# Kernel tuning notes

Hardware: AMD Instinct MI355X
Metric: run time of the kernel (lower is better)

Reference implementation:

```python
import jax, jax.numpy as jnp
import numpy as np

P_DROP = 0.25
DROP_KEY_SEED = 42  # fixed seed makes dropout deterministic for baseline comparison


def setup_inputs() -> dict:
    key = jax.random.key(0)
    k1, k2, k3, k4 = jax.random.split(key, 4)
    B, S, D, DV = 16, 2048, 64, 512
    x1 = jax.random.normal(k1, (B, S, D), dtype=jnp.float32)   # queries [B,S,64]
    m = jax.random.normal(k2, (D, DV), dtype=jnp.float32)      # [64,512]
    n = jax.random.normal(k3, (S, DV), dtype=jnp.float32)      # [S,512]
    q = jax.random.normal(k4, (S, DV), dtype=jnp.float32)      # values [S,512]
    return {"x1": x1, "m": m, "n": n, "q": q}


def reference(x1, m, n, q):
    scale = jnp.float32(1.0 / 64.0)  # hard-coded in original (not 1/sqrt(d))
    kT = jnp.matmul(m, n.T)                        # matmul5: [64, S]
    scores = jnp.matmul(x1, kT) * scale            # [B, S, S]
    probs = jax.nn.softmax(scores, axis=-1)        # softmax over last dim
    keep = jax.random.bernoulli(jax.random.key(DROP_KEY_SEED), 1.0 - P_DROP, probs.shape)
    probs = jnp.where(keep, probs / (1.0 - P_DROP), jnp.float32(0.0))  # dropout (train mode)
    return jnp.matmul(probs, q)                    # [B, S, DV]
```

## Files before the change

### kernel.cpp

```cpp
#include <hip/hip_runtime.h>


typedef short  s8v __attribute__((ext_vector_type(8)));
typedef float  f4v __attribute__((ext_vector_type(4)));

__device__ __forceinline__ unsigned short f2bf(float f) {
  unsigned int u = __float_as_uint(f);
  u += 0x7fffu + ((u >> 16) & 1u);
  return (unsigned short)(u >> 16);
}
__device__ __forceinline__ float bf2f(unsigned short h) {
  return __uint_as_float(((unsigned int)h) << 16);
}

__device__ __forceinline__ unsigned int rotl(unsigned int x, unsigned int r) {
  return __builtin_amdgcn_alignbit(x, x, 32u - r);
}

__device__ __forceinline__ unsigned int jax_bits(unsigned int idx) {
  const unsigned int K0 = 0u, K1 = 42u, K2 = 0x1BD11BDAu ^ K0 ^ K1;
  unsigned int x0 = 0u, x1 = idx;
  x0 += K0; x1 += K1;
#define TF_R(r) { x0 += x1; x1 = rotl(x1, r); x1 ^= x0; }
  TF_R(13) TF_R(15) TF_R(26) TF_R(6)
  x0 += K1; x1 += K2 + 1u;
  TF_R(17) TF_R(29) TF_R(16) TF_R(24)
  x0 += K2; x1 += K0 + 2u;
  TF_R(13) TF_R(15) TF_R(26) TF_R(6)
  x0 += K0; x1 += K1 + 3u;
  TF_R(17) TF_R(29) TF_R(16) TF_R(24)
  x0 += K1; x1 += K2 + 4u;
  TF_R(13) TF_R(15) TF_R(26) TF_R(6)
  x0 += K2; x1 += K0 + 5u;
#undef TF_R
  return x0 ^ x1;
}

__device__ __forceinline__ f4v mfma16(s8v a, s8v b, f4v c) {
  return __builtin_amdgcn_mfma_f32_16x16x32_bf16(a, b, c, 0, 0, 0);
}

__global__ void prep_all(const float* __restrict__ x1, const float* __restrict__ q,
                         const float* __restrict__ m, const float* __restrict__ nmat,
                         unsigned short* __restrict__ Xhi, unsigned short* __restrict__ qT,
                         unsigned short* __restrict__ Khi, unsigned short* __restrict__ Klo) {
  const int blk = blockIdx.x;
  const int t = threadIdx.x;
  if (blk < 512) {
    __shared__ float Lm[64][68];
    const int s = blk * 4 + (t >> 6);
    const int d = t & 63;
    float a0 = 0.f, a1 = 0.f, a2 = 0.f, a3 = 0.f;
    for (int ch = 0; ch < 8; ++ch) {
      const int dv0 = ch * 64;
      __syncthreads();
#pragma unroll
      for (int k = 0; k < 4; ++k) {
        const int fi = t + k * 256;
        const int row = fi >> 4, c4 = fi & 15;
        *(float4*)&Lm[row][c4 * 4] =
            *(const float4*)&m[(size_t)row * 512 + dv0 + c4 * 4];
      }
      __syncthreads();
      const float4* nv = (const float4*)&nmat[(size_t)s * 512 + dv0];
#pragma unroll
      for (int j4 = 0; j4 < 16; ++j4) {
        const float4 nf = nv[j4];
        const float4 mf = *(const float4*)&Lm[d][j4 * 4];
        a0 = fmaf(mf.x, nf.x, a0); a1 = fmaf(mf.y, nf.y, a1);
        a2 = fmaf(mf.z, nf.z, a2); a3 = fmaf(mf.w, nf.w, a3);
      }
    }
    const float kv = ((a0 + a1) + (a2 + a3)) * (1.44269504088896340736f / 64.0f);
    const unsigned short h = f2bf(kv);
    Khi[s * 64 + d] = h;
    Klo[s * 64 + d] = f2bf(kv - bf2f(h));
  } else if (blk < 1536) {
    const int i = ((blk - 512) * 256 + t) * 8;
    float4 a = *(const float4*)&x1[i];
    float4 b = *(const float4*)&x1[i + 4];
    ushort4 o0, o1;
    o0.x = f2bf(a.x); o0.y = f2bf(a.y); o0.z = f2bf(a.z); o0.w = f2bf(a.w);
    o1.x = f2bf(b.x); o1.y = f2bf(b.y); o1.z = f2bf(b.z); o1.w = f2bf(b.w);
    *(ushort4*)&Xhi[i] = o0;
    *(ushort4*)&Xhi[i + 4] = o1;
  } else {
    __shared__ unsigned short tile[64][65];
    const int bb = blk - 1536;
    const int s0 = (bb >> 3) * 64;
    const int d0 = (bb & 7) * 64;
#pragma unroll
    for (int k = 0; k < 16; ++k) {
      int lin = t + k * 256;
      int r = lin >> 6, c = lin & 63;
      tile[c][r] = f2bf(q[(size_t)(s0 + r) * 512 + d0 + c]);
    }
    __syncthreads();
#pragma unroll
    for (int k = 0; k < 16; ++k) {
      int lin = t + k * 256;
      int rr = lin >> 6, cc = lin & 63;
      qT[(size_t)(d0 + rr) * 2048 + s0 + cc] = tile[rr][cc];
    }
  }
}

__global__ __launch_bounds__(512, 4) void attn_main(
    const unsigned short* __restrict__ Xhi,
    const unsigned short* __restrict__ Khi, const unsigned short* __restrict__ Klo,
    const unsigned short* __restrict__ qT, float* __restrict__ out) {
  __shared__ unsigned short Xs[64][72];
  __shared__ unsigned short Ps[2][64][136];
  __shared__ float rsum[8][64];

  const int tid  = threadIdx.x;
  const int wave = tid >> 6;
  const int lane = tid & 63;
  const int l15  = lane & 15;
  const int quad = lane >> 4;

  const int b    = blockIdx.x >> 5;
  const int row0 = (blockIdx.x & 31) * 64;

  {
    const int r = tid >> 3, c8 = (tid & 7) * 8;
    *(uint4*)&Xs[r][c8] =
        *(const uint4*)&Xhi[((size_t)(b * 2048 + row0 + r)) * 64 + c8];
  }

  const unsigned short* __restrict__ khp = Khi + ((wave * 16 + l15) * 64 + quad * 8);
  const unsigned short* __restrict__ klp = Klo + ((wave * 16 + l15) * 64 + quad * 8);
  const unsigned short* __restrict__ qvp = qT + ((wave * 64 + l15) * 2048 + quad * 8);

  s8v Kh0 = *(const s8v*)(khp);
  s8v Kh1 = *(const s8v*)(khp + 32);
  s8v Kl0 = *(const s8v*)(klp);
  s8v Kl1 = *(const s8v*)(klp + 32);

  f4v acc[4][4];
#pragma unroll
  for (int mt = 0; mt < 4; ++mt)
#pragma unroll
    for (int nt = 0; nt < 4; ++nt) acc[mt][nt] = f4v{0.f, 0.f, 0.f, 0.f};
  float rs[4] = {0.f, 0.f, 0.f, 0.f};

  const unsigned int idxl =
      ((unsigned int)(b * 2048 + row0 + l15)) * 2048u +
      (unsigned int)(wave * 16 + quad * 4);

  __syncthreads();

  for (int it = 0; it < 16; ++it) {
    const int kt = it * 128;
    unsigned short (*Pb)[136] = Ps[it & 1];

#pragma unroll
    for (int nt = 0; nt < 4; ++nt) {
      const s8v Xb0 = *(const s8v*)&Xs[nt * 16 + l15][quad * 8];
      const s8v Xb1 = *(const s8v*)&Xs[nt * 16 + l15][quad * 8 + 32];
      f4v c = {0.f, 0.f, 0.f, 0.f};
      c = mfma16(Kh0, Xb0, c);  c = mfma16(Kh1, Xb1, c);
      c = mfma16(Kl0, Xb0, c);  c = mfma16(Kl1, Xb1, c);
      const unsigned int idx0 = idxl + (unsigned int)(nt * 32768 + kt);
      float p[4];
#pragma unroll
      for (int r = 0; r < 4; ++r) {
        float e = exp2f(c[r]);
        rs[nt] += e;
        const unsigned int bits = jax_bits(idx0 + r);
        p[r] = (bits < 0xC0000000u) ? e : 0.0f;
      }
      unsigned int p01, p23;
      asm("v_cvt_pk_bf16_f32 %0, %1, %2" : "=v"(p01) : "v"(p[0]), "v"(p[1]));
      asm("v_cvt_pk_bf16_f32 %0, %1, %2" : "=v"(p23) : "v"(p[2]), "v"(p[3]));
      *(uint2*)&Pb[nt * 16 + l15][wave * 16 + quad * 4] = make_uint2(p01, p23);
    }

    if (it < 15) {
      const int ko = (it + 1) * 8192;
      Kh0 = *(const s8v*)(khp + ko);
      Kh1 = *(const s8v*)(khp + ko + 32);
      Kl0 = *(const s8v*)(klp + ko);
      Kl1 = *(const s8v*)(klp + ko + 32);
    }

    __syncthreads();

#pragma unroll
    for (int ks = 0; ks < 4; ++ks) {
      s8v Va[4];
#pragma unroll
      for (int mt = 0; mt < 4; ++mt)
        Va[mt] = *(const s8v*)(qvp + mt * (16 * 2048) + kt + ks * 32);
      __builtin_amdgcn_s_setprio(1);
#pragma unroll
      for (int nt = 0; nt < 4; ++nt) {
        const s8v Pf = *(const s8v*)&Pb[nt * 16 + l15][ks * 32 + quad * 8];
#pragma unroll
        for (int mt = 0; mt < 4; ++mt) acc[mt][nt] = mfma16(Va[mt], Pf, acc[mt][nt]);
      }
      __builtin_amdgcn_s_setprio(0);
    }
  }

#pragma unroll
  for (int nt = 0; nt < 4; ++nt) {
    float v = rs[nt];
    v += __shfl_xor(v, 16);
    v += __shfl_xor(v, 32);
    if (quad == 0) rsum[wave][nt * 16 + l15] = v;
  }
  __syncthreads();

#pragma unroll
  for (int nt = 0; nt < 4; ++nt) {
    const int rloc = nt * 16 + l15;
    float tot = 0.f;
#pragma unroll
    for (int w2 = 0; w2 < 8; ++w2) tot += rsum[w2][rloc];
    const float inv = 1.0f / (0.75f * tot);
    const size_t base = ((size_t)(b * 2048 + row0 + rloc)) * 512 + wave * 64;
#pragma unroll
    for (int mt = 0; mt < 4; ++mt) {
      f4v v = acc[mt][nt];
      v[0] *= inv; v[1] *= inv; v[2] *= inv; v[3] *= inv;
      *(f4v*)&out[base + mt * 16 + quad * 4] = v;
    }
  }
}

extern "C" void kernel_launch(void* const* d_in, const int* in_sizes, int n_in,
                              void* d_out, int out_size, void* d_ws, size_t ws_size,
                              hipStream_t stream) {
  (void)in_sizes; (void)n_in; (void)out_size; (void)ws_size;
  const float* x1 = (const float*)d_in[0];
  const float* m  = (const float*)d_in[1];
  const float* n  = (const float*)d_in[2];
  const float* q  = (const float*)d_in[3];
  float* out = (float*)d_out;

  char* ws = (char*)d_ws;
  unsigned short* Khi = (unsigned short*)(ws);
  unsigned short* Klo = (unsigned short*)(ws + 262144);
  unsigned short* Xhi = (unsigned short*)(ws + 524288);
  unsigned short* qT  = (unsigned short*)(ws + 4718592);

  prep_all<<<1792, 256, 0, stream>>>(x1, q, m, n, Xhi, qT, Khi, Klo);
  attn_main<<<512, 512, 0, stream>>>(Xhi, Khi, Klo, qT, out);
}
```

Measured before the change: 312.3 us.

## Software-pipeline QK/softmax of next tile with PV of current tile

Restructures the main loop so the score/exp/dropout computation for tile it+1 is issued before the P·V MFMAs of tile it, using the double-buffered P tiles, with a single barrier per iteration. This lets the VALU-heavy Threefry dropout work overlap with the matrix-core work instead of running in separate phases. It also drops the s_setprio hints and replaces __syncthreads with a manual lgkmcnt wait plus barrier and a sched_barrier. The risk is higher register pressure from live K fragments alongside the accumulators, and a redundant K reload on the last iterations.

```diff
diff --git a/kernel.cpp b/kernel.cpp
--- a/kernel.cpp
+++ b/kernel.cpp
@@ -132,11 +132,7 @@
   const unsigned short* __restrict__ klp = Klo + ((wave * 16 + l15) * 64 + quad * 8);
   const unsigned short* __restrict__ qvp = qT + ((wave * 64 + l15) * 2048 + quad * 8);
 
-  s8v Kh0 = *(const s8v*)(khp);
-  s8v Kh1 = *(const s8v*)(khp + 32);
-  s8v Kl0 = *(const s8v*)(klp);
-  s8v Kl1 = *(const s8v*)(klp + 32);
-
+  s8v Kh0, Kh1, Kl0, Kl1;
   f4v acc[4][4];
 #pragma unroll
   for (int mt = 0; mt < 4; ++mt)
@@ -148,12 +144,17 @@
       ((unsigned int)(b * 2048 + row0 + l15)) * 2048u +
       (unsigned int)(wave * 16 + quad * 4);
 
-  __syncthreads();
-
-  for (int it = 0; it < 16; ++it) {
-    const int kt = it * 128;
-    unsigned short (*Pb)[136] = Ps[it & 1];
-
+  auto KLOAD = [&](int itk) {
+    const int ko = itk * 8192;
+    Kh0 = *(const s8v*)(khp + ko);
+    Kh1 = *(const s8v*)(khp + ko + 32);
+    Kl0 = *(const s8v*)(klp + ko);
+    Kl1 = *(const s8v*)(klp + ko + 32);
+  };
+
+  auto QK = [&](int itn) {
+    unsigned short (*Pn)[136] = Ps[itn & 1];
+    const int ktn = itn * 128;
 #pragma unroll
     for (int nt = 0; nt < 4; ++nt) {
       const s8v Xb0 = *(const s8v*)&Xs[nt * 16 + l15][quad * 8];
@@ -161,7 +162,7 @@
       f4v c = {0.f, 0.f, 0.f, 0.f};
       c = mfma16(Kh0, Xb0, c);  c = mfma16(Kh1, Xb1, c);
       c = mfma16(Kl0, Xb0, c);  c = mfma16(Kl1, Xb1, c);
-      const unsigned int idx0 = idxl + (unsigned int)(nt * 32768 + kt);
+      const unsigned int idx0 = idxl + (unsigned int)(nt * 32768 + ktn);
       float p[4];
 #pragma unroll
       for (int r = 0; r < 4; ++r) {
@@ -173,35 +174,47 @@
       unsigned int p01, p23;
       asm("v_cvt_pk_bf16_f32 %0, %1, %2" : "=v"(p01) : "v"(p[0]), "v"(p[1]));
       asm("v_cvt_pk_bf16_f32 %0, %1, %2" : "=v"(p23) : "v"(p[2]), "v"(p[3]));
-      *(uint2*)&Pb[nt * 16 + l15][wave * 16 + quad * 4] = make_uint2(p01, p23);
-    }
-
-    if (it < 15) {
-      const int ko = (it + 1) * 8192;
-      Kh0 = *(const s8v*)(khp + ko);
-      Kh1 = *(const s8v*)(khp + ko + 32);
-      Kl0 = *(const s8v*)(klp + ko);
-      Kl1 = *(const s8v*)(klp + ko + 32);
-    }
-
-    __syncthreads();
-
+      *(uint2*)&Pn[nt * 16 + l15][wave * 16 + quad * 4] = make_uint2(p01, p23);
+    }
+  };
+
+  auto PV = [&](int it) {
+    unsigned short (*Pc)[136] = Ps[it & 1];
+    const int kt = it * 128;
 #pragma unroll
     for (int ks = 0; ks < 4; ++ks) {
       s8v Va[4];
 #pragma unroll
       for (int mt = 0; mt < 4; ++mt)
         Va[mt] = *(const s8v*)(qvp + mt * (16 * 2048) + kt + ks * 32);
-      __builtin_amdgcn_s_setprio(1);
 #pragma unroll
       for (int nt = 0; nt < 4; ++nt) {
-        const s8v Pf = *(const s8v*)&Pb[nt * 16 + l15][ks * 32 + quad * 8];
+        const s8v Pf = *(const s8v*)&Pc[nt * 16 + l15][ks * 32 + quad * 8];
 #pragma unroll
         for (int mt = 0; mt < 4; ++mt) acc[mt][nt] = mfma16(Va[mt], Pf, acc[mt][nt]);
       }
-      __builtin_amdgcn_s_setprio(0);
-    }
-  }
+    }
+  };
+
+  auto bar = [&]() {
+    asm volatile("s_waitcnt lgkmcnt(0)" ::: "memory");
+    __builtin_amdgcn_s_barrier();
+    __builtin_amdgcn_sched_barrier(0);
+  };
+
+  KLOAD(0);
+  __syncthreads();
+  QK(0);
+  KLOAD(1);
+  bar();
+
+  for (int it = 0; it < 15; ++it) {
+    QK(it + 1);
+    KLOAD(it + 2 < 16 ? it + 2 : 15);
+    PV(it);
+    bar();
+  }
+  PV(15);
 
 #pragma unroll
   for (int nt = 0; nt < 4; ++nt) {
```

Result: no change. 317.3 us (+1.6%).

## Precompute dropout bitmask in prep kernel instead of hashing inside attention loop

Applied to the files above, without the earlier changes.

Adds a prep-stage block range that evaluates the Threefry-based dropout RNG for every score element and packs the keep decisions into a 32-bit-per-word bitmask in workspace. The attention kernel then loads one mask word per tile row and tests bits instead of running the 20-round hash inline. This takes heavy integer ALU work and register pressure out of the main loop's critical path. In exchange it adds a 16 MB mask write and read and many more prep blocks.

```diff
diff --git a/kernel.cpp b/kernel.cpp
--- a/kernel.cpp
+++ b/kernel.cpp
@@ -43,7 +43,8 @@
 __global__ void prep_all(const float* __restrict__ x1, const float* __restrict__ q,
                          const float* __restrict__ m, const float* __restrict__ nmat,
                          unsigned short* __restrict__ Xhi, unsigned short* __restrict__ qT,
-                         unsigned short* __restrict__ Khi, unsigned short* __restrict__ Klo) {
+                         unsigned short* __restrict__ Khi, unsigned short* __restrict__ Klo,
+                         unsigned int* __restrict__ mask) {
   const int blk = blockIdx.x;
   const int t = threadIdx.x;
   if (blk < 512) {
@@ -84,7 +85,7 @@
     o1.x = f2bf(b.x); o1.y = f2bf(b.y); o1.z = f2bf(b.z); o1.w = f2bf(b.w);
     *(ushort4*)&Xhi[i] = o0;
     *(ushort4*)&Xhi[i + 4] = o1;
-  } else {
+  } else if (blk < 1792) {
     __shared__ unsigned short tile[64][65];
     const int bb = blk - 1536;
     const int s0 = (bb >> 3) * 64;
@@ -102,13 +103,23 @@
       int rr = lin >> 6, cc = lin & 63;
       qT[(size_t)(d0 + rr) * 2048 + s0 + cc] = tile[rr][cc];
     }
+  } else {
+    const int i = (blk - 1792) * 256 + t;
+    const unsigned int e0 = (unsigned int)i * 32u;
+    unsigned int w = 0u;
+#pragma unroll 4
+    for (int j = 0; j < 32; ++j) {
+      w |= (jax_bits(e0 + (unsigned int)j) < 0xC0000000u ? 1u : 0u) << j;
+    }
+    mask[i] = w;
   }
 }
 
 __global__ __launch_bounds__(512, 4) void attn_main(
     const unsigned short* __restrict__ Xhi,
     const unsigned short* __restrict__ Khi, const unsigned short* __restrict__ Klo,
-    const unsigned short* __restrict__ qT, float* __restrict__ out) {
+    const unsigned short* __restrict__ qT, const unsigned int* __restrict__ mask,
+    float* __restrict__ out) {
   __shared__ unsigned short Xs[64][72];
   __shared__ unsigned short Ps[2][64][136];
   __shared__ float rsum[8][64];
@@ -132,6 +143,11 @@
   const unsigned short* __restrict__ klp = Klo + ((wave * 16 + l15) * 64 + quad * 8);
   const unsigned short* __restrict__ qvp = qT + ((wave * 64 + l15) * 2048 + quad * 8);
 
+  const int wc = wave * 16 + quad * 4;
+  const unsigned int mshift = (unsigned int)(wc & 31);
+  const unsigned int* __restrict__ maskp =
+      mask + ((size_t)(b * 2048 + row0 + l15) * 64 + (wc >> 5));
+
   s8v Kh0 = *(const s8v*)(khp);
   s8v Kh1 = *(const s8v*)(khp + 32);
   s8v Kl0 = *(const s8v*)(klp);
@@ -144,15 +160,16 @@
     for (int nt = 0; nt < 4; ++nt) acc[mt][nt] = f4v{0.f, 0.f, 0.f, 0.f};
   float rs[4] = {0.f, 0.f, 0.f, 0.f};
 
-  const unsigned int idxl =
-      ((unsigned int)(b * 2048 + row0 + l15)) * 2048u +
-      (unsigned int)(wave * 16 + quad * 4);
-
   __syncthreads();
 
   for (int it = 0; it < 16; ++it) {
     const int kt = it * 128;
     unsigned short (*Pb)[136] = Ps[it & 1];
+
+    unsigned int mw[4];
+#pragma unroll
+    for (int nt = 0; nt < 4; ++nt)
+      mw[nt] = maskp[nt * 1024 + it * 4];
 
 #pragma unroll
     for (int nt = 0; nt < 4; ++nt) {
@@ -161,14 +178,12 @@
       f4v c = {0.f, 0.f, 0.f, 0.f};
       c = mfma16(Kh0, Xb0, c);  c = mfma16(Kh1, Xb1, c);
       c = mfma16(Kl0, Xb0, c);  c = mfma16(Kl1, Xb1, c);
-      const unsigned int idx0 = idxl + (unsigned int)(nt * 32768 + kt);
       float p[4];
 #pragma unroll
       for (int r = 0; r < 4; ++r) {
         float e = exp2f(c[r]);
         rs[nt] += e;
-        const unsigned int bits = jax_bits(idx0 + r);
-        p[r] = (bits < 0xC0000000u) ? e : 0.0f;
+        p[r] = ((mw[nt] >> (mshift + r)) & 1u) ? e : 0.0f;
       }
       unsigned int p01, p23;
       asm("v_cvt_pk_bf16_f32 %0, %1, %2" : "=v"(p01) : "v"(p[0]), "v"(p[1]));
@@ -240,11 +255,12 @@
   float* out = (float*)d_out;
 
   char* ws = (char*)d_ws;
-  unsigned short* Khi = (unsigned short*)(ws);
-  unsigned short* Klo = (unsigned short*)(ws + 262144);
-  unsigned short* Xhi = (unsigned short*)(ws + 524288);
-  unsigned short* qT  = (unsigned short*)(ws + 4718592);
-
-  prep_all<<<1792, 256, 0, stream>>>(x1, q, m, n, Xhi, qT, Khi, Klo);
-  attn_main<<<512, 512, 0, stream>>>(Xhi, Khi, Klo, qT, out);
-}
+  unsigned short* Khi  = (unsigned short*)(ws);
+  unsigned short* Klo  = (unsigned short*)(ws + 262144);
+  unsigned short* Xhi  = (unsigned short*)(ws + 524288);
+  unsigned short* qT   = (unsigned short*)(ws + 4718592);
+  unsigned int*   mask = (unsigned int*)(ws + 6815744);
+
+  prep_all<<<9984, 256, 0, stream>>>(x1, q, m, n, Xhi, qT, Khi, Klo, mask);
+  attn_main<<<512, 512, 0, stream>>>(Xhi, Khi, Klo, qT, mask, out);
+}
```

After: 396.7 us. +27.0%, slower.

## Retile attention kernel to 32-row blocks with 4 waves each

Applied to the files above, without the earlier changes.

Halves the query rows per block and the waves per block, doubling the grid, and gives each wave more keys and output columns. Each wave now builds 2 score tiles per key group and accumulates an 8x2 tile of output fragments. The K prefetch across iterations and the staging of V fragments in registers are dropped in favour of loads inside the loop. The intent is more, smaller blocks for better occupancy and balance, at the cost of less reuse of V fragments across query tiles and more exposed load latency.

```diff
diff --git a/kernel.cpp b/kernel.cpp
--- a/kernel.cpp
+++ b/kernel.cpp
@@ -105,13 +105,13 @@
   }
 }
 
-__global__ __launch_bounds__(512, 4) void attn_main(
+__global__ __launch_bounds__(256, 4) void attn_main(
     const unsigned short* __restrict__ Xhi,
     const unsigned short* __restrict__ Khi, const unsigned short* __restrict__ Klo,
     const unsigned short* __restrict__ qT, float* __restrict__ out) {
-  __shared__ unsigned short Xs[64][72];
-  __shared__ unsigned short Ps[2][64][136];
-  __shared__ float rsum[8][64];
+  __shared__ unsigned short Xs[32][72];
+  __shared__ unsigned short Ps[2][32][136];
+  __shared__ float rsum[4][32];
 
   const int tid  = threadIdx.x;
   const int wave = tid >> 6;
@@ -119,8 +119,8 @@
   const int l15  = lane & 15;
   const int quad = lane >> 4;
 
-  const int b    = blockIdx.x >> 5;
-  const int row0 = (blockIdx.x & 31) * 64;
+  const int b    = blockIdx.x >> 6;
+  const int row0 = (blockIdx.x & 63) * 32;
 
   {
     const int r = tid >> 3, c8 = (tid & 7) * 8;
@@ -128,83 +128,79 @@
         *(const uint4*)&Xhi[((size_t)(b * 2048 + row0 + r)) * 64 + c8];
   }
 
-  const unsigned short* __restrict__ khp = Khi + ((wave * 16 + l15) * 64 + quad * 8);
-  const unsigned short* __restrict__ klp = Klo + ((wave * 16 + l15) * 64 + quad * 8);
-  const unsigned short* __restrict__ qvp = qT + ((wave * 64 + l15) * 2048 + quad * 8);
-
-  s8v Kh0 = *(const s8v*)(khp);
-  s8v Kh1 = *(const s8v*)(khp + 32);
-  s8v Kl0 = *(const s8v*)(klp);
-  s8v Kl1 = *(const s8v*)(klp + 32);
-
-  f4v acc[4][4];
-#pragma unroll
-  for (int mt = 0; mt < 4; ++mt)
-#pragma unroll
-    for (int nt = 0; nt < 4; ++nt) acc[mt][nt] = f4v{0.f, 0.f, 0.f, 0.f};
-  float rs[4] = {0.f, 0.f, 0.f, 0.f};
+  const unsigned short* __restrict__ khp0 = Khi + ((wave * 32 + l15) * 64 + quad * 8);
+  const unsigned short* __restrict__ klp0 = Klo + ((wave * 32 + l15) * 64 + quad * 8);
+  const unsigned short* __restrict__ khp1 = khp0 + 16 * 64;
+  const unsigned short* __restrict__ klp1 = klp0 + 16 * 64;
+  const unsigned short* __restrict__ qvp = qT + ((wave * 128 + l15) * 2048 + quad * 8);
+
+  f4v acc[8][2];
+#pragma unroll
+  for (int mt = 0; mt < 8; ++mt)
+#pragma unroll
+    for (int nt = 0; nt < 2; ++nt) acc[mt][nt] = f4v{0.f, 0.f, 0.f, 0.f};
+  float rs[2] = {0.f, 0.f};
 
   const unsigned int idxl =
       ((unsigned int)(b * 2048 + row0 + l15)) * 2048u +
-      (unsigned int)(wave * 16 + quad * 4);
+      (unsigned int)(wave * 32 + quad * 4);
 
   __syncthreads();
 
   for (int it = 0; it < 16; ++it) {
     const int kt = it * 128;
+    const int ko = it * 8192;
     unsigned short (*Pb)[136] = Ps[it & 1];
 
 #pragma unroll
-    for (int nt = 0; nt < 4; ++nt) {
-      const s8v Xb0 = *(const s8v*)&Xs[nt * 16 + l15][quad * 8];
-      const s8v Xb1 = *(const s8v*)&Xs[nt * 16 + l15][quad * 8 + 32];
-      f4v c = {0.f, 0.f, 0.f, 0.f};
-      c = mfma16(Kh0, Xb0, c);  c = mfma16(Kh1, Xb1, c);
-      c = mfma16(Kl0, Xb0, c);  c = mfma16(Kl1, Xb1, c);
-      const unsigned int idx0 = idxl + (unsigned int)(nt * 32768 + kt);
-      float p[4];
-#pragma unroll
-      for (int r = 0; r < 4; ++r) {
-        float e = exp2f(c[r]);
-        rs[nt] += e;
-        const unsigned int bits = jax_bits(idx0 + r);
-        p[r] = (bits < 0xC0000000u) ? e : 0.0f;
-      }
-      unsigned int p01, p23;
-      asm("v_cvt_pk_bf16_f32 %0, %1, %2" : "=v"(p01) : "v"(p[0]), "v"(p[1]));
-      asm("v_cvt_pk_bf16_f32 %0, %1, %2" : "=v"(p23) : "v"(p[2]), "v"(p[3]));
-      *(uint2*)&Pb[nt * 16 + l15][wave * 16 + quad * 4] = make_uint2(p01, p23);
-    }
-
-    if (it < 15) {
-      const int ko = (it + 1) * 8192;
-      Kh0 = *(const s8v*)(khp + ko);
-      Kh1 = *(const s8v*)(khp + ko + 32);
-      Kl0 = *(const s8v*)(klp + ko);
-      Kl1 = *(const s8v*)(klp + ko + 32);
+    for (int kg = 0; kg < 2; ++kg) {
+      const s8v Kh0 = *(const s8v*)((kg ? khp1 : khp0) + ko);
+      const s8v Kh1 = *(const s8v*)((kg ? khp1 : khp0) + ko + 32);
+      const s8v Kl0 = *(const s8v*)((kg ? klp1 : klp0) + ko);
+      const s8v Kl1 = *(const s8v*)((kg ? klp1 : klp0) + ko + 32);
+#pragma unroll
+      for (int nt = 0; nt < 2; ++nt) {
+        const s8v Xb0 = *(const s8v*)&Xs[nt * 16 + l15][quad * 8];
+        const s8v Xb1 = *(const s8v*)&Xs[nt * 16 + l15][quad * 8 + 32];
+        f4v c = {0.f, 0.f, 0.f, 0.f};
+        c = mfma16(Kh0, Xb0, c);  c = mfma16(Kh1, Xb1, c);
+        c = mfma16(Kl0, Xb0, c);  c = mfma16(Kl1, Xb1, c);
+        const unsigned int idx0 =
+            idxl + (unsigned int)(nt * 32768 + kt + kg * 16);
+        float p[4];
+#pragma unroll
+        for (int r = 0; r < 4; ++r) {
+          float e = exp2f(c[r]);
+          rs[nt] += e;
+          const unsigned int bits = jax_bits(idx0 + r);
+          p[r] = (bits < 0xC0000000u) ? e : 0.0f;
+        }
+        unsigned int p01, p23;
+        asm("v_cvt_pk_bf16_f32 %0, %1, %2" : "=v"(p01) : "v"(p[0]), "v"(p[1]));
+        asm("v_cvt_pk_bf16_f32 %0, %1, %2" : "=v"(p23) : "v"(p[2]), "v"(p[3]));
+        *(uint2*)&Pb[nt * 16 + l15][wave * 32 + kg * 16 + quad * 4] =
+            make_uint2(p01, p23);
+      }
     }
 
     __syncthreads();
 
 #pragma unroll
     for (int ks = 0; ks < 4; ++ks) {
-      s8v Va[4];
-#pragma unroll
-      for (int mt = 0; mt < 4; ++mt)
-        Va[mt] = *(const s8v*)(qvp + mt * (16 * 2048) + kt + ks * 32);
-      __builtin_amdgcn_s_setprio(1);
-#pragma unroll
-      for (int nt = 0; nt < 4; ++nt) {
+#pragma unroll
+      for (int nt = 0; nt < 2; ++nt) {
         const s8v Pf = *(const s8v*)&Pb[nt * 16 + l15][ks * 32 + quad * 8];
 #pragma unroll
-        for (int mt = 0; mt < 4; ++mt) acc[mt][nt] = mfma16(Va[mt], Pf, acc[mt][nt]);
-      }
-      __builtin_amdgcn_s_setprio(0);
-    }
-  }
-
-#pragma unroll
-  for (int nt = 0; nt < 4; ++nt) {
+        for (int mt = 0; mt < 8; ++mt) {
+          const s8v Va = *(const s8v*)(qvp + mt * (16 * 2048) + kt + ks * 32);
+          acc[mt][nt] = mfma16(Va, Pf, acc[mt][nt]);
+        }
+      }
+    }
+  }
+
+#pragma unroll
+  for (int nt = 0; nt < 2; ++nt) {
     float v = rs[nt];
     v += __shfl_xor(v, 16);
     v += __shfl_xor(v, 32);
@@ -213,15 +209,13 @@
   __syncthreads();
 
 #pragma unroll
-  for (int nt = 0; nt < 4; ++nt) {
+  for (int nt = 0; nt < 2; ++nt) {
     const int rloc = nt * 16 + l15;
-    float tot = 0.f;
-#pragma unroll
-    for (int w2 = 0; w2 < 8; ++w2) tot += rsum[w2][rloc];
+    const float tot = rsum[0][rloc] + rsum[1][rloc] + rsum[2][rloc] + rsum[3][rloc];
     const float inv = 1.0f / (0.75f * tot);
-    const size_t base = ((size_t)(b * 2048 + row0 + rloc)) * 512 + wave * 64;
-#pragma unroll
-    for (int mt = 0; mt < 4; ++mt) {
+    const size_t base = ((size_t)(b * 2048 + row0 + rloc)) * 512 + wave * 128;
+#pragma unroll
+    for (int mt = 0; mt < 8; ++mt) {
       f4v v = acc[mt][nt];
       v[0] *= inv; v[1] *= inv; v[2] *= inv; v[3] *= inv;
       *(f4v*)&out[base + mt * 16 + quad * 4] = v;
@@ -246,5 +240,5 @@
   unsigned short* qT  = (unsigned short*)(ws + 4718592);
 
   prep_all<<<1792, 256, 0, stream>>>(x1, q, m, n, Xhi, qT, Khi, Klo);
-  attn_main<<<512, 512, 0, stream>>>(Xhi, Khi, Klo, qT, out);
-}
+  attn_main<<<1024, 256, 0, stream>>>(Xhi, Khi, Klo, qT, out);
+}
```

Measured after the change: 415.4 us. 33.0% more time.
